# Kernel tuning notes

Hardware: AMD Instinct MI355X
Metric: run time of the kernel (lower is better)

The kernel has to match this reference:

```python
import jax, jax.numpy as jnp
import numpy as np

T, S, F, A, POS = 32, 4096, 256, 64, 128


def setup_inputs() -> dict:
    key = jax.random.key(0)
    ks = jax.random.split(key, 12)
    sc = lambda fan_in: 1.0 / np.sqrt(fan_in)
    return {
        "batch_data": jax.random.normal(ks[0], (T * S, F), dtype=jnp.float32),
        "xywh": jax.random.uniform(ks[1], (T * S, 4), dtype=jnp.float32),
        # nn.Linear params (y = x @ W.T + b)
        "Wa": jax.random.uniform(ks[2], (A, F), minval=-sc(F), maxval=sc(F)),
        "ba": jax.random.uniform(ks[3], (A,), minval=-sc(F), maxval=sc(F)),
        "Wb": jax.random.uniform(ks[4], (A, F), minval=-sc(F), maxval=sc(F)),
        "bb": jax.random.uniform(ks[5], (A,), minval=-sc(F), maxval=sc(F)),
        "Wg": jax.random.uniform(ks[6], (F, F), minval=-sc(F), maxval=sc(F)),
        "bg": jax.random.uniform(ks[7], (F,), minval=-sc(F), maxval=sc(F)),
        "Wh": jax.random.uniform(ks[8], (POS, 2), minval=-sc(2), maxval=sc(2)),
        "bh": jax.random.uniform(ks[9], (POS,), minval=-sc(2), maxval=sc(2)),
    }


def reference(batch_data, xywh, Wa, ba, Wb, bb, Wg, bg, Wh, bh):
    x = batch_data.reshape(T, S, F)
    pos = xywh.reshape(T, S, -1)
    # positional embedding path (computed in original forward but unused in output)
    avg_pos = jnp.mean(pos, axis=0)            # [S, 4]
    rel_pos = pos[:, :, :2] - avg_pos[:, :2]   # [T, S, 2]
    _pos_embeds = rel_pos @ Wh.T + bh          # [T, S, POS] (dead, matches source)

    theta = x @ Wa.T + ba                      # [T, S, A]
    phi = x @ Wb.T + bb                        # [T, S, A]
    feats = x @ Wg.T + bg                      # [T, S, F]

    # per-object temporal attention: attn[s, t, u] = theta[t, s] . phi[u, s]
    attn = jnp.einsum('tsa,usa->stu', theta, phi)       # [S, T, T]
    out = jnp.einsum('stu,usf->tsf', attn, feats)       # [T, S, F]
    return out
```

## Files before the change

### kernel.cpp

```cpp
#include <hip/hip_runtime.h>

#define T_ 32
#define S_ 4096
#define F_ 256
#define A_ 64
#define NS 2

typedef __attribute__((ext_vector_type(8))) short s8v;
typedef __attribute__((ext_vector_type(4))) float f4v;
typedef __attribute__((ext_vector_type(4))) short s4v;

#define MFMA(a, b, c) __builtin_amdgcn_mfma_f32_16x16x32_bf16((a), (b), (c), 0, 0, 0)

__device__ __forceinline__ unsigned short f2bf(float f) {
    unsigned int u = __builtin_bit_cast(unsigned int, f);
    u += 0x7FFFu + ((u >> 16) & 1u);
    return (unsigned short)(u >> 16);
}

__global__ void convert_weights(const float* __restrict__ Wa,
                                const float* __restrict__ Wb,
                                const float* __restrict__ Wg,
                                unsigned short* __restrict__ wsB)
{
    int base = (blockIdx.x * 256 + threadIdx.x) * 4;
    const float* src;
    if (base < 16384)      src = Wa + base;
    else if (base < 32768) src = Wb + (base - 16384);
    else                   src = Wg + (base - 32768);
    float4 v = *(const float4*)src;
    s4v p;
    p[0] = (short)f2bf(v.x); p[1] = (short)f2bf(v.y);
    p[2] = (short)f2bf(v.z); p[3] = (short)f2bf(v.w);
    *(s4v*)(wsB + base) = p;
}

#define XS_OFF 0
#define TH_OFF 32768
#define PH_OFF 40960
#define AT_OFF 49152
#define FT_OFF 32768
#define LDS_BYTES 53248

__global__ __launch_bounds__(256, 3) void fused_temporal(
    const float* __restrict__ X,
    const unsigned short* __restrict__ wsB,
    const float* __restrict__ ba, const float* __restrict__ bb,
    const float* __restrict__ bg,
    float* __restrict__ out)
{
    __shared__ alignas(16) unsigned char smem[LDS_BYTES];
    const int tid  = threadIdx.x;
    const int wave = tid >> 6;
    const int lane = tid & 63;
    const int quad = lane >> 4;
    const int l15  = lane & 15;
    const int s0   = blockIdx.x * NS;

    const unsigned short* WaB = wsB;
    const unsigned short* WbB = wsB + 16384;
    const unsigned short* WgB = wsB + 32768;

    #pragma unroll
    for (int i = 0; i < 8; ++i) {
        int linear = i * 256 + tid;
        int r = linear >> 5;
        int c = linear & 31;
        int t  = r & 31;
        int sl = r >> 5;
        const float* xp = X + ((size_t)(t * S_ + s0 + sl)) * F_ + c * 8;
        float4 v0 = *(const float4*)(xp);
        float4 v1 = *(const float4*)(xp + 4);
        s8v p;
        p[0] = (short)f2bf(v0.x); p[1] = (short)f2bf(v0.y);
        p[2] = (short)f2bf(v0.z); p[3] = (short)f2bf(v0.w);
        p[4] = (short)f2bf(v1.x); p[5] = (short)f2bf(v1.y);
        p[6] = (short)f2bf(v1.z); p[7] = (short)f2bf(v1.w);
        *(s8v*)(&smem[XS_OFF + r * 512 + (((c + r) & 31) << 4)]) = p;
    }
    __syncthreads();

    s8v wg[2][8];
    {
        const int n0 = 16 * wave;
        s8v wafrag[8], wbfrag[8];
        {
            const unsigned short* wa_row = WaB + (size_t)(n0 + l15) * F_ + quad * 8;
            const unsigned short* wb_row = WbB + (size_t)(n0 + l15) * F_ + quad * 8;
            #pragma unroll
            for (int ks = 0; ks < 8; ++ks) {
                wafrag[ks] = *(const s8v*)(wa_row + ks * 32);
                wbfrag[ks] = *(const s8v*)(wb_row + ks * 32);
            }
        }

        f4v ta[4], pa[4];
        #pragma unroll
        for (int mt = 0; mt < 4; ++mt) { ta[mt] = f4v{0.f,0.f,0.f,0.f}; pa[mt] = f4v{0.f,0.f,0.f,0.f}; }

        #pragma unroll
        for (int ks = 0; ks < 8; ++ks) {
            int chunk = 4 * ks + quad;
            #pragma unroll
            for (int mt = 0; mt < 4; ++mt) {
                int r = 16 * mt + l15;
                s8v a = *(const s8v*)(&smem[XS_OFF + r * 512 + (((chunk + r) & 31) << 4)]);
                ta[mt] = MFMA(a, wafrag[ks], ta[mt]);
                pa[mt] = MFMA(a, wbfrag[ks], pa[mt]);
            }
        }

        #pragma unroll
        for (int g = 0; g < 2; ++g) {
            const unsigned short* wg_row = WgB + (size_t)(64 * wave + 16 * g + l15) * F_ + quad * 8;
            #pragma unroll
            for (int ks = 0; ks < 8; ++ks) wg[g][ks] = *(const s8v*)(wg_row + ks * 32);
        }

        float biasa = ba[n0 + l15];
        float biasb = bb[n0 + l15];
        int a_col = n0 + l15;
        int chunk = a_col >> 3;
        int sub   = (a_col & 7) * 2;
        #pragma unroll
        for (int mt = 0; mt < 4; ++mt) {
            #pragma unroll
            for (int r = 0; r < 4; ++r) {
                int row = 16 * mt + quad * 4 + r;
                int sw  = ((chunk + row) & 7) << 4;
                *(unsigned short*)(&smem[TH_OFF + row * 128 + sw + sub]) = f2bf(ta[mt][r] + biasa);
                *(unsigned short*)(&smem[PH_OFF + row * 128 + sw + sub]) = f2bf(pa[mt][r] + biasb);
            }
        }
    }
    __syncthreads();

    {
        int sl  = wave >> 1;
        int mt2 = wave & 1;
        int t2  = l15 + 16 * mt2;
        int rth = sl * 32 + t2;
        #pragma unroll
        for (int nt2 = 0; nt2 < 2; ++nt2) {
            int u2  = l15 + 16 * nt2;
            int rph = sl * 32 + u2;
            f4v acc2 = {0.f,0.f,0.f,0.f};
            #pragma unroll
            for (int ks = 0; ks < 2; ++ks) {
                int chunk = 4 * ks + quad;
                s8v av = *(const s8v*)(&smem[TH_OFF + rth * 128 + (((chunk + rth) & 7) << 4)]);
                s8v bv = *(const s8v*)(&smem[PH_OFF + rph * 128 + (((chunk + rph) & 7) << 4)]);
                acc2 = MFMA(av, bv, acc2);
            }
            int chunk = u2 >> 3;
            int sub   = (u2 & 7) * 2;
            #pragma unroll
            for (int r = 0; r < 4; ++r) {
                int tt  = quad * 4 + r + 16 * mt2;
                int rat = sl * 32 + tt;
                *(unsigned short*)(&smem[AT_OFF + rat * 64 + (((chunk + rat) & 3) << 4) + sub]) = f2bf(acc2[r]);
            }
        }
    }
    __syncthreads();

    {
        s8v battn[2][2];
        #pragma unroll
        for (int sl = 0; sl < 2; ++sl) {
            #pragma unroll
            for (int nt = 0; nt < 2; ++nt) {
                int rat = sl * 32 + l15 + 16 * nt;
                battn[sl][nt] = *(const s8v*)(&smem[AT_OFF + rat * 64 + (((quad + rat) & 3) << 4)]);
            }
        }

        const int ftbase = FT_OFF + wave * 2048;

        #pragma unroll
        for (int g = 0; g < 4; ++g) {
            int n0 = 64 * wave + 16 * g;
            f4v fa[4];
            #pragma unroll
            for (int mt = 0; mt < 4; ++mt) fa[mt] = f4v{0.f,0.f,0.f,0.f};
            #pragma unroll
            for (int ks = 0; ks < 8; ++ks) {
                int chunk = 4 * ks + quad;
                #pragma unroll
                for (int mt = 0; mt < 4; ++mt) {
                    int r = 16 * mt + l15;
                    s8v a = *(const s8v*)(&smem[XS_OFF + r * 512 + (((chunk + r) & 31) << 4)]);
                    fa[mt] = MFMA(a, wg[g & 1][ks], fa[mt]);
                }
            }
            if (g < 2) {
                const unsigned short* wg_row = WgB + (size_t)(64 * wave + 16 * (g + 2) + l15) * F_ + quad * 8;
                #pragma unroll
                for (int ks = 0; ks < 8; ++ks) wg[g & 1][ks] = *(const s8v*)(wg_row + ks * 32);
            }

            float biasg = bg[n0 + l15];
            #pragma unroll
            for (int mt = 0; mt < 4; ++mt) {
                int sl = mt >> 1;
                int u0 = (mt & 1) * 16 + quad * 4;
                s4v pk;
                #pragma unroll
                for (int r = 0; r < 4; ++r) pk[r] = (short)f2bf(fa[mt][r] + biasg);
                int addr = ftbase + sl * 1024 + l15 * 64 + ((((u0 >> 3) + l15) & 3) << 4) + (u0 & 7) * 2;
                *(s4v*)(&smem[addr]) = pk;
            }

            int f0 = n0 + 4 * quad;
            #pragma unroll
            for (int sl = 0; sl < 2; ++sl) {
                s8v avf = *(const s8v*)(&smem[ftbase + sl * 1024 + l15 * 64 + (((quad + l15) & 3) << 4)]);
                #pragma unroll
                for (int nt = 0; nt < 2; ++nt) {
                    f4v z = {0.f,0.f,0.f,0.f};
                    f4v acc = MFMA(avf, battn[sl][nt], z);
                    int t = l15 + 16 * nt;
                    float4 st;
                    st.x = acc[0]; st.y = acc[1]; st.z = acc[2]; st.w = acc[3];
                    *(float4*)(out + ((size_t)(t * S_ + s0 + sl)) * F_ + f0) = st;
                }
            }
        }
    }
}

extern "C" void kernel_launch(void* const* d_in, const int* in_sizes, int n_in,
                              void* d_out, int out_size, void* d_ws, size_t ws_size,
                              hipStream_t stream) {
    (void)in_sizes; (void)n_in; (void)ws_size; (void)out_size;
    const float* X  = (const float*)d_in[0];
    const float* Wa = (const float*)d_in[2];
    const float* ba = (const float*)d_in[3];
    const float* Wb = (const float*)d_in[4];
    const float* bb = (const float*)d_in[5];
    const float* Wg = (const float*)d_in[6];
    const float* bg = (const float*)d_in[7];
    float* out = (float*)d_out;
    unsigned short* wsB = (unsigned short*)d_ws;

    convert_weights<<<dim3(96), dim3(256), 0, stream>>>(Wa, Wb, Wg, wsB);
    fused_temporal<<<dim3(S_ / NS), dim3(256), 0, stream>>>(X, wsB, ba, bb, bg, out);
}
```

Measured before the change: 314.6 us.

## Make fused kernel persistent with double-buffered X prefetch and LDS-resident weights

Turns the one-block-per-object-pair kernel into a persistent kernel of 256 blocks that each loop over several object pairs. Each block loads Wa/Wb into LDS and keeps all of Wg in registers once, so weights are no longer reloaded from global memory per block. The next X tile is prefetched into registers while the current one is computed, then written into a second LDS buffer. The gains are lower weight traffic and overlap of load latency with compute. The cost is one block per CU with about 148KB of LDS and high register pressure, which can leave little latency hiding and limits scheduling to 256 blocks.

```diff
diff --git a/kernel.cpp b/kernel.cpp
--- a/kernel.cpp
+++ b/kernel.cpp
@@ -5,6 +5,8 @@
 #define F_ 256
 #define A_ 64
 #define NS 2
+#define GRID 256
+#define ITERS (S_ / NS / GRID)
 
 typedef __attribute__((ext_vector_type(8))) short s8v;
 typedef __attribute__((ext_vector_type(4))) float f4v;
@@ -35,14 +37,22 @@
     *(s4v*)(wsB + base) = p;
 }
 
-#define XS_OFF 0
-#define TH_OFF 32768
-#define PH_OFF 40960
-#define AT_OFF 49152
-#define FT_OFF 32768
-#define LDS_BYTES 53248
-
-__global__ __launch_bounds__(256, 3) void fused_temporal(
+#define X0_OFF 0
+#define X1_OFF 32768
+#define WW_OFF 65536
+#define TH_OFF 131072
+#define PH_OFF 139264
+#define AT_OFF 147456
+#define FT_OFF TH_OFF
+#define LDS_BYTES 151552
+
+#define BAR() do {                                            \
+    asm volatile("s_waitcnt lgkmcnt(0)" ::: "memory");        \
+    __builtin_amdgcn_s_barrier();                             \
+    __builtin_amdgcn_sched_barrier(0);                        \
+} while (0)
+
+__global__ __launch_bounds__(256, 1) void fused_temporal(
     const float* __restrict__ X,
     const unsigned short* __restrict__ wsB,
     const float* __restrict__ ba, const float* __restrict__ bb,
@@ -55,177 +65,211 @@
     const int lane = tid & 63;
     const int quad = lane >> 4;
     const int l15  = lane & 15;
-    const int s0   = blockIdx.x * NS;
-
-    const unsigned short* WaB = wsB;
-    const unsigned short* WbB = wsB + 16384;
+    const int b    = blockIdx.x;
+
     const unsigned short* WgB = wsB + 32768;
 
     #pragma unroll
-    for (int i = 0; i < 8; ++i) {
-        int linear = i * 256 + tid;
-        int r = linear >> 5;
-        int c = linear & 31;
-        int t  = r & 31;
-        int sl = r >> 5;
-        const float* xp = X + ((size_t)(t * S_ + s0 + sl)) * F_ + c * 8;
-        float4 v0 = *(const float4*)(xp);
-        float4 v1 = *(const float4*)(xp + 4);
-        s8v p;
-        p[0] = (short)f2bf(v0.x); p[1] = (short)f2bf(v0.y);
-        p[2] = (short)f2bf(v0.z); p[3] = (short)f2bf(v0.w);
-        p[4] = (short)f2bf(v1.x); p[5] = (short)f2bf(v1.y);
-        p[6] = (short)f2bf(v1.z); p[7] = (short)f2bf(v1.w);
-        *(s8v*)(&smem[XS_OFF + r * 512 + (((c + r) & 31) << 4)]) = p;
-    }
-    __syncthreads();
-
-    s8v wg[2][8];
+    for (int i = 0; i < 16; ++i) {
+        int cid = i * 256 + tid;
+        int r = cid >> 5, c = cid & 31;
+        s8v v = *(const s8v*)(wsB + (size_t)cid * 8);
+        *(s8v*)(&smem[WW_OFF + r * 512 + (((c + r) & 31) << 4)]) = v;
+    }
+    s8v wg[4][8];
+    #pragma unroll
+    for (int g = 0; g < 4; ++g) {
+        const unsigned short* p = WgB + (size_t)(64 * wave + 16 * g + l15) * F_ + quad * 8;
+        #pragma unroll
+        for (int ks = 0; ks < 8; ++ks) wg[g][ks] = *(const s8v*)(p + ks * 32);
+    }
     {
-        const int n0 = 16 * wave;
-        s8v wafrag[8], wbfrag[8];
+        int s0 = b * NS;
+        #pragma unroll
+        for (int i = 0; i < 8; ++i) {
+            int linear = i * 256 + tid;
+            int r = linear >> 5, c = linear & 31;
+            int t = r & 31, sl = r >> 5;
+            const float* xp = X + ((size_t)(t * S_ + s0 + sl)) * F_ + c * 8;
+            float4 v0 = *(const float4*)(xp);
+            float4 v1 = *(const float4*)(xp + 4);
+            s8v p;
+            p[0] = (short)f2bf(v0.x); p[1] = (short)f2bf(v0.y);
+            p[2] = (short)f2bf(v0.z); p[3] = (short)f2bf(v0.w);
+            p[4] = (short)f2bf(v1.x); p[5] = (short)f2bf(v1.y);
+            p[6] = (short)f2bf(v1.z); p[7] = (short)f2bf(v1.w);
+            *(s8v*)(&smem[X0_OFF + r * 512 + (((c + r) & 31) << 4)]) = p;
+        }
+    }
+    float biasa = ba[16 * wave + l15];
+    float biasb = bb[16 * wave + l15];
+    BAR();
+
+    float4 xnx[16];
+    #pragma unroll 1
+    for (int it = 0; it < ITERS; ++it) {
+        const int xs = (it & 1) ? X1_OFF : X0_OFF;
+        const int xd = (it & 1) ? X0_OFF : X1_OFF;
+        const int s0 = (it * GRID + b) * NS;
+
+        if (it + 1 < ITERS) {
+            int sn = ((it + 1) * GRID + b) * NS;
+            #pragma unroll
+            for (int i = 0; i < 8; ++i) {
+                int linear = i * 256 + tid;
+                int r = linear >> 5, c = linear & 31;
+                int t = r & 31, sl = r >> 5;
+                const float* xp = X + ((size_t)(t * S_ + sn + sl)) * F_ + c * 8;
+                xnx[2 * i]     = *(const float4*)(xp);
+                xnx[2 * i + 1] = *(const float4*)(xp + 4);
+            }
+        }
+
         {
-            const unsigned short* wa_row = WaB + (size_t)(n0 + l15) * F_ + quad * 8;
-            const unsigned short* wb_row = WbB + (size_t)(n0 + l15) * F_ + quad * 8;
-            #pragma unroll
-            for (int ks = 0; ks < 8; ++ks) {
-                wafrag[ks] = *(const s8v*)(wa_row + ks * 32);
-                wbfrag[ks] = *(const s8v*)(wb_row + ks * 32);
-            }
-        }
-
-        f4v ta[4], pa[4];
-        #pragma unroll
-        for (int mt = 0; mt < 4; ++mt) { ta[mt] = f4v{0.f,0.f,0.f,0.f}; pa[mt] = f4v{0.f,0.f,0.f,0.f}; }
-
-        #pragma unroll
-        for (int ks = 0; ks < 8; ++ks) {
-            int chunk = 4 * ks + quad;
-            #pragma unroll
-            for (int mt = 0; mt < 4; ++mt) {
-                int r = 16 * mt + l15;
-                s8v a = *(const s8v*)(&smem[XS_OFF + r * 512 + (((chunk + r) & 31) << 4)]);
-                ta[mt] = MFMA(a, wafrag[ks], ta[mt]);
-                pa[mt] = MFMA(a, wbfrag[ks], pa[mt]);
-            }
-        }
-
-        #pragma unroll
-        for (int g = 0; g < 2; ++g) {
-            const unsigned short* wg_row = WgB + (size_t)(64 * wave + 16 * g + l15) * F_ + quad * 8;
-            #pragma unroll
-            for (int ks = 0; ks < 8; ++ks) wg[g][ks] = *(const s8v*)(wg_row + ks * 32);
-        }
-
-        float biasa = ba[n0 + l15];
-        float biasb = bb[n0 + l15];
-        int a_col = n0 + l15;
-        int chunk = a_col >> 3;
-        int sub   = (a_col & 7) * 2;
-        #pragma unroll
-        for (int mt = 0; mt < 4; ++mt) {
-            #pragma unroll
-            for (int r = 0; r < 4; ++r) {
-                int row = 16 * mt + quad * 4 + r;
-                int sw  = ((chunk + row) & 7) << 4;
-                *(unsigned short*)(&smem[TH_OFF + row * 128 + sw + sub]) = f2bf(ta[mt][r] + biasa);
-                *(unsigned short*)(&smem[PH_OFF + row * 128 + sw + sub]) = f2bf(pa[mt][r] + biasb);
-            }
-        }
-    }
-    __syncthreads();
-
-    {
-        int sl  = wave >> 1;
-        int mt2 = wave & 1;
-        int t2  = l15 + 16 * mt2;
-        int rth = sl * 32 + t2;
-        #pragma unroll
-        for (int nt2 = 0; nt2 < 2; ++nt2) {
-            int u2  = l15 + 16 * nt2;
-            int rph = sl * 32 + u2;
-            f4v acc2 = {0.f,0.f,0.f,0.f};
-            #pragma unroll
-            for (int ks = 0; ks < 2; ++ks) {
-                int chunk = 4 * ks + quad;
-                s8v av = *(const s8v*)(&smem[TH_OFF + rth * 128 + (((chunk + rth) & 7) << 4)]);
-                s8v bv = *(const s8v*)(&smem[PH_OFF + rph * 128 + (((chunk + rph) & 7) << 4)]);
-                acc2 = MFMA(av, bv, acc2);
-            }
-            int chunk = u2 >> 3;
-            int sub   = (u2 & 7) * 2;
-            #pragma unroll
-            for (int r = 0; r < 4; ++r) {
-                int tt  = quad * 4 + r + 16 * mt2;
-                int rat = sl * 32 + tt;
-                *(unsigned short*)(&smem[AT_OFF + rat * 64 + (((chunk + rat) & 3) << 4) + sub]) = f2bf(acc2[r]);
-            }
-        }
-    }
-    __syncthreads();
-
-    {
-        s8v battn[2][2];
-        #pragma unroll
-        for (int sl = 0; sl < 2; ++sl) {
-            #pragma unroll
-            for (int nt = 0; nt < 2; ++nt) {
-                int rat = sl * 32 + l15 + 16 * nt;
-                battn[sl][nt] = *(const s8v*)(&smem[AT_OFF + rat * 64 + (((quad + rat) & 3) << 4)]);
-            }
-        }
-
-        const int ftbase = FT_OFF + wave * 2048;
-
-        #pragma unroll
-        for (int g = 0; g < 4; ++g) {
-            int n0 = 64 * wave + 16 * g;
-            f4v fa[4];
-            #pragma unroll
-            for (int mt = 0; mt < 4; ++mt) fa[mt] = f4v{0.f,0.f,0.f,0.f};
+            const int n0 = 16 * wave;
+            const int ra = n0 + l15;
+            const int rb = 64 + n0 + l15;
+            f4v ta[4], pa[4];
+            #pragma unroll
+            for (int mt = 0; mt < 4; ++mt) { ta[mt] = f4v{0.f,0.f,0.f,0.f}; pa[mt] = f4v{0.f,0.f,0.f,0.f}; }
             #pragma unroll
             for (int ks = 0; ks < 8; ++ks) {
                 int chunk = 4 * ks + quad;
+                s8v bfa = *(const s8v*)(&smem[WW_OFF + ra * 512 + (((chunk + ra) & 31) << 4)]);
+                s8v bfb = *(const s8v*)(&smem[WW_OFF + rb * 512 + (((chunk + rb) & 31) << 4)]);
                 #pragma unroll
                 for (int mt = 0; mt < 4; ++mt) {
                     int r = 16 * mt + l15;
-                    s8v a = *(const s8v*)(&smem[XS_OFF + r * 512 + (((chunk + r) & 31) << 4)]);
-                    fa[mt] = MFMA(a, wg[g & 1][ks], fa[mt]);
-                }
-            }
-            if (g < 2) {
-                const unsigned short* wg_row = WgB + (size_t)(64 * wave + 16 * (g + 2) + l15) * F_ + quad * 8;
-                #pragma unroll
-                for (int ks = 0; ks < 8; ++ks) wg[g & 1][ks] = *(const s8v*)(wg_row + ks * 32);
-            }
-
-            float biasg = bg[n0 + l15];
+                    s8v a = *(const s8v*)(&smem[xs + r * 512 + (((chunk + r) & 31) << 4)]);
+                    ta[mt] = MFMA(a, bfa, ta[mt]);
+                    pa[mt] = MFMA(a, bfb, pa[mt]);
+                }
+            }
+            int a_col = n0 + l15;
+            int chunk = a_col >> 3;
+            int sub   = (a_col & 7) * 2;
             #pragma unroll
             for (int mt = 0; mt < 4; ++mt) {
-                int sl = mt >> 1;
-                int u0 = (mt & 1) * 16 + quad * 4;
-                s4v pk;
-                #pragma unroll
-                for (int r = 0; r < 4; ++r) pk[r] = (short)f2bf(fa[mt][r] + biasg);
-                int addr = ftbase + sl * 1024 + l15 * 64 + ((((u0 >> 3) + l15) & 3) << 4) + (u0 & 7) * 2;
-                *(s4v*)(&smem[addr]) = pk;
-            }
-
-            int f0 = n0 + 4 * quad;
+                #pragma unroll
+                for (int r = 0; r < 4; ++r) {
+                    int row = 16 * mt + quad * 4 + r;
+                    int sw  = ((chunk + row) & 7) << 4;
+                    *(unsigned short*)(&smem[TH_OFF + row * 128 + sw + sub]) = f2bf(ta[mt][r] + biasa);
+                    *(unsigned short*)(&smem[PH_OFF + row * 128 + sw + sub]) = f2bf(pa[mt][r] + biasb);
+                }
+            }
+        }
+        BAR();
+
+        {
+            int sl  = wave >> 1;
+            int mt2 = wave & 1;
+            int t2  = l15 + 16 * mt2;
+            int rth = sl * 32 + t2;
+            #pragma unroll
+            for (int nt2 = 0; nt2 < 2; ++nt2) {
+                int u2  = l15 + 16 * nt2;
+                int rph = sl * 32 + u2;
+                f4v acc2 = {0.f,0.f,0.f,0.f};
+                #pragma unroll
+                for (int ks = 0; ks < 2; ++ks) {
+                    int chunk = 4 * ks + quad;
+                    s8v av = *(const s8v*)(&smem[TH_OFF + rth * 128 + (((chunk + rth) & 7) << 4)]);
+                    s8v bv = *(const s8v*)(&smem[PH_OFF + rph * 128 + (((chunk + rph) & 7) << 4)]);
+                    acc2 = MFMA(av, bv, acc2);
+                }
+                int chunk = u2 >> 3;
+                int sub   = (u2 & 7) * 2;
+                #pragma unroll
+                for (int r = 0; r < 4; ++r) {
+                    int tt  = quad * 4 + r + 16 * mt2;
+                    int rat = sl * 32 + tt;
+                    *(unsigned short*)(&smem[AT_OFF + rat * 64 + (((chunk + rat) & 3) << 4) + sub]) = f2bf(acc2[r]);
+                }
+            }
+        }
+        BAR();
+
+        {
+            s8v battn[2][2];
             #pragma unroll
             for (int sl = 0; sl < 2; ++sl) {
-                s8v avf = *(const s8v*)(&smem[ftbase + sl * 1024 + l15 * 64 + (((quad + l15) & 3) << 4)]);
                 #pragma unroll
                 for (int nt = 0; nt < 2; ++nt) {
-                    f4v z = {0.f,0.f,0.f,0.f};
-                    f4v acc = MFMA(avf, battn[sl][nt], z);
-                    int t = l15 + 16 * nt;
-                    float4 st;
-                    st.x = acc[0]; st.y = acc[1]; st.z = acc[2]; st.w = acc[3];
-                    *(float4*)(out + ((size_t)(t * S_ + s0 + sl)) * F_ + f0) = st;
-                }
-            }
-        }
+                    int rat = sl * 32 + l15 + 16 * nt;
+                    battn[sl][nt] = *(const s8v*)(&smem[AT_OFF + rat * 64 + (((quad + rat) & 3) << 4)]);
+                }
+            }
+            const int ftbase = FT_OFF + wave * 2048;
+
+            f4v fa[4][4];
+            #pragma unroll
+            for (int g = 0; g < 4; ++g)
+                #pragma unroll
+                for (int mt = 0; mt < 4; ++mt) fa[g][mt] = f4v{0.f,0.f,0.f,0.f};
+            #pragma unroll
+            for (int ks = 0; ks < 8; ++ks) {
+                int chunk = 4 * ks + quad;
+                s8v a[4];
+                #pragma unroll
+                for (int mt = 0; mt < 4; ++mt) {
+                    int r = 16 * mt + l15;
+                    a[mt] = *(const s8v*)(&smem[xs + r * 512 + (((chunk + r) & 31) << 4)]);
+                }
+                #pragma unroll
+                for (int g = 0; g < 4; ++g)
+                    #pragma unroll
+                    for (int mt = 0; mt < 4; ++mt)
+                        fa[g][mt] = MFMA(a[mt], wg[g][ks], fa[g][mt]);
+            }
+
+            #pragma unroll
+            for (int g = 0; g < 4; ++g) {
+                int n0 = 64 * wave + 16 * g;
+                float biasg = bg[n0 + l15];
+                #pragma unroll
+                for (int mt = 0; mt < 4; ++mt) {
+                    int sl = mt >> 1;
+                    int u0 = (mt & 1) * 16 + quad * 4;
+                    s4v pk;
+                    #pragma unroll
+                    for (int r = 0; r < 4; ++r) pk[r] = (short)f2bf(fa[g][mt][r] + biasg);
+                    int addr = ftbase + sl * 1024 + l15 * 64 + ((((u0 >> 3) + l15) & 3) << 4) + (u0 & 7) * 2;
+                    *(s4v*)(&smem[addr]) = pk;
+                }
+                int f0 = n0 + 4 * quad;
+                #pragma unroll
+                for (int sl = 0; sl < 2; ++sl) {
+                    s8v avf = *(const s8v*)(&smem[ftbase + sl * 1024 + l15 * 64 + (((quad + l15) & 3) << 4)]);
+                    #pragma unroll
+                    for (int nt = 0; nt < 2; ++nt) {
+                        f4v z = {0.f,0.f,0.f,0.f};
+                        f4v acc = MFMA(avf, battn[sl][nt], z);
+                        int t = l15 + 16 * nt;
+                        float4 st;
+                        st.x = acc[0]; st.y = acc[1]; st.z = acc[2]; st.w = acc[3];
+                        *(float4*)(out + ((size_t)(t * S_ + s0 + sl)) * F_ + f0) = st;
+                    }
+                }
+            }
+        }
+
+        if (it + 1 < ITERS) {
+            #pragma unroll
+            for (int i = 0; i < 8; ++i) {
+                int linear = i * 256 + tid;
+                int r = linear >> 5, c = linear & 31;
+                float4 v0 = xnx[2 * i];
+                float4 v1 = xnx[2 * i + 1];
+                s8v p;
+                p[0] = (short)f2bf(v0.x); p[1] = (short)f2bf(v0.y);
+                p[2] = (short)f2bf(v0.z); p[3] = (short)f2bf(v0.w);
+                p[4] = (short)f2bf(v1.x); p[5] = (short)f2bf(v1.y);
+                p[6] = (short)f2bf(v1.z); p[7] = (short)f2bf(v1.w);
+                *(s8v*)(&smem[xd + r * 512 + (((c + r) & 31) << 4)]) = p;
+            }
+        }
+        BAR();
     }
 }
 
@@ -244,5 +288,5 @@
     unsigned short* wsB = (unsigned short*)d_ws;
 
     convert_weights<<<dim3(96), dim3(256), 0, stream>>>(Wa, Wb, Wg, wsB);
-    fused_temporal<<<dim3(S_ / NS), dim3(256), 0, stream>>>(X, wsB, ba, bb, bg, out);
-}
+    fused_temporal<<<dim3(GRID), dim3(256), 0, stream>>>(X, wsB, ba, bb, bg, out);
+}
```

Result: faster. 305.0 us (-3.0%).
